# Kernel optimization log

Hardware: AMD Instinct MI355X
Metric: run time of the kernel (lower is better)

The kernel has to match this reference:

```python
import jax, jax.numpy as jnp
import numpy as np

B = 128
J = 22
Q = J * 4          # 88
R = 3
C = 4
H = 512            # LSTM hidden
ENC = 256 * 3      # 768 concatenated encoder outputs
STATE_IN = Q + R + C   # 95
OFF_IN = Q + R         # 91
OUT = Q + R + C        # 95


def _linear_params(key, fan_in, fan_out):
    kw, kb = jax.random.split(key)
    s = 1.0 / np.sqrt(fan_in)
    w = jax.random.uniform(kw, (fan_in, fan_out), jnp.float32, -s, s)
    b = jax.random.uniform(kb, (fan_out,), jnp.float32, -s, s)
    return w, b


def setup_inputs() -> dict:
    key = jax.random.key(0)
    ks = jax.random.split(key, 24)
    inp = {
        "past_root_vel": jax.random.normal(ks[0], (B, 10, R)) * 0.1,
        "past_quats": jax.random.normal(ks[1], (B, 10, Q)),
        "past_root_offset": jax.random.normal(ks[2], (B, 10, R)),
        "past_quat_offset": jax.random.normal(ks[3], (B, 10, Q)),
        "past_contacts": jax.random.uniform(ks[4], (B, 10, C)),
        "target_root_pos": jax.random.normal(ks[5], (B, R)),
        "target_quats": jax.random.normal(ks[6], (B, Q)),
        "init_root_pos": jax.random.normal(ks[7], (B, R)),
        "pred_weights": jax.random.normal(ks[8], (B, 4 * H, ENC + H)) * 0.03,
        "pred_bias": jax.random.normal(ks[9], (B, 4 * H)) * 0.01,
    }
    inp["se_w1"], inp["se_b1"] = _linear_params(ks[10], STATE_IN, 512)
    inp["se_w2"], inp["se_b2"] = _linear_params(ks[11], 512, 256)
    inp["oe_w1"], inp["oe_b1"] = _linear_params(ks[12], OFF_IN, 512)
    inp["oe_w2"], inp["oe_b2"] = _linear_params(ks[13], 512, 256)
    inp["te_w1"], inp["te_b1"] = _linear_params(ks[14], Q, 512)
    inp["te_w2"], inp["te_b2"] = _linear_params(ks[15], 512, 256)
    inp["de_w1"], inp["de_b1"] = _linear_params(ks[16], H, 512)
    inp["de_w2"], inp["de_b2"] = _linear_params(ks[17], 512, 256)
    inp["de_w3"], inp["de_b3"] = _linear_params(ks[18], 256, OUT)
    return inp


def reference(past_root_vel, past_quats, past_root_offset, past_quat_offset,
              past_contacts, target_root_pos, target_quats, init_root_pos,
              pred_weights, pred_bias,
              se_w1, se_b1, se_w2, se_b2,
              oe_w1, oe_b1, oe_w2, oe_b2,
              te_w1, te_b1, te_w2, te_b2,
              de_w1, de_b1, de_w2, de_b2, de_w3, de_b3):
    b = past_quats.shape[0]

    def enc(x, w1, b1, w2, b2):
        return jax.nn.relu(jax.nn.relu(x @ w1 + b1) @ w2 + b2)

    # target encoding is identical every step; hoist it
    h_target = enc(target_quats, te_w1, te_b1, te_w2, te_b2)

    def step(root_vel, quats, root_offset, quat_offset, contacts, h, c):
        state_vec = jnp.concatenate([contacts, quats, root_vel], axis=1)
        offset_vec = jnp.concatenate([root_offset, quat_offset], axis=1)
        h_state = enc(state_vec, se_w1, se_b1, se_w2, se_b2)
        h_offset = enc(offset_vec, oe_w1, oe_b1, oe_w2, oe_b2)
        pred_in = jnp.concatenate([h_state, h_offset, h_target], axis=1)  # [B,768]
        # per-sample hypernetwork LSTM cell (torch gate order i,f,g,o)
        z = jnp.concatenate([pred_in, h], axis=1)  # [B, 1280]
        gates = jnp.einsum('boi,bi->bo', pred_weights, z) + pred_bias
        i_g, f_g, g_g, o_g = jnp.split(gates, 4, axis=1)
        c2 = jax.nn.sigmoid(f_g) * c + jax.nn.sigmoid(i_g) * jnp.tanh(g_g)
        h2 = jax.nn.sigmoid(o_g) * jnp.tanh(c2)
        # decoder (512,512,256,out), no activation on last layer
        d = jax.nn.relu(h2 @ de_w1 + de_b1)
        d = jax.nn.relu(d @ de_w2 + de_b2)
        out = d @ de_w3 + de_b3
        next_quats = out[:, :Q] + quats
        next_rvel = out[:, Q:Q + R] + root_vel
        next_contacts = jax.nn.sigmoid(out[:, Q + R:])
        nq = next_quats.reshape(b, Q // 4, 4)
        nq = nq / jnp.maximum(jnp.linalg.norm(nq, axis=2, keepdims=True), 1e-12)
        return next_rvel, nq.reshape(b, Q), next_contacts, h2, c2

    h0 = jnp.zeros((b, H), past_quats.dtype)
    c0 = jnp.zeros((b, H), past_quats.dtype)

    def past_body(carry, x):
        glob, h, c, _, _, _, _, _ = carry
        rvel, quats, roff, qoff, cont = x
        nrv, nq, nc, h2, c2 = step(rvel, quats, roff, qoff, cont, h, c)
        glob2 = glob + rvel
        nroff = glob2 - target_root_pos
        nqoff = nq - target_quats
        return (glob2, h2, c2, nrv, nq, nc, nroff, nqoff), None

    z3 = jnp.zeros((b, R), past_quats.dtype)
    init = (init_root_pos, h0, c0, z3,
            jnp.zeros((b, Q), past_quats.dtype),
            jnp.zeros((b, C), past_quats.dtype),
            z3, jnp.zeros((b, Q), past_quats.dtype))
    xs = (jnp.swapaxes(past_root_vel, 0, 1), jnp.swapaxes(past_quats, 0, 1),
          jnp.swapaxes(past_root_offset, 0, 1), jnp.swapaxes(past_quat_offset, 0, 1),
          jnp.swapaxes(past_contacts, 0, 1))
    carry, _ = jax.lax.scan(past_body, init, xs)
    glob, h, c, nrv, nq, nc, roff, qoff = carry

    first_frame = jnp.concatenate([nrv, nq], axis=1)  # NOTE: rvel not glob, as in source

    def trans_body(carry, _):
        glob, h, c, rvel, quats, cont, roff, qoff = carry
        nrv, nq, nc, h2, c2 = step(rvel, quats, roff, qoff, cont, h, c)
        glob2 = glob + nrv
        nroff = glob2 - target_root_pos
        nqoff = nq - target_quats
        pose = jnp.concatenate([glob2, nq], axis=1)
        return (glob2, h2, c2, nrv, nq, nc, nroff, nqoff), (pose, nc)

    carry2 = (glob, h, c, nrv, nq, nc, roff, qoff)
    _, (poses, conts) = jax.lax.scan(trans_body, carry2, None, length=29)

    pred_poses = jnp.concatenate([first_frame[:, None], jnp.swapaxes(poses, 0, 1)], axis=1)
    pred_contacts = jnp.concatenate([nc[:, None], jnp.swapaxes(conts, 0, 1)], axis=1)
    return pred_poses, pred_contacts
```

## Files before the change

kernel.cpp:

```cpp
#include <hip/hip_runtime.h>
#include <hip/hip_bf16.h>
#include <math.h>

#define BATCH 128
#define QD 88
#define HDIM 512
#define ZDIM 1280
#define GDIM 2048
#define PROW 1536
#define QSTRIDE 6144
#define NPAST 10
#define NTRANS 29
#define NSTEPS (NPAST + NTRANS)
#define OUTD 95
#define POSE_ELEMS (BATCH * 30 * 91)

typedef float f32x4 __attribute__((ext_vector_type(4)));
typedef unsigned int u32x4 __attribute__((ext_vector_type(4)));

__device__ __forceinline__ float sig_(float x) { return 1.0f / (1.0f + expf(-x)); }
__device__ __forceinline__ void dot4_(const uint4 wv, const float4 zv, float& d) {
    const float4 f = *(const float4*)&wv;
    d = fmaf(f.x, zv.x, d); d = fmaf(f.y, zv.y, d);
    d = fmaf(f.z, zv.z, d); d = fmaf(f.w, zv.w, d);
}
__device__ __forceinline__ void fma4_(float4& acc, float x, const float4 w) {
    acc.x = fmaf(x, w.x, acc.x); acc.y = fmaf(x, w.y, acc.y);
    acc.z = fmaf(x, w.z, acc.z); acc.w = fmaf(x, w.w, acc.w);
}
__device__ __forceinline__ unsigned q12_(float w, float inv) {
    const unsigned u = __float2uint_rn(fmaf(w, inv, 2048.0f));
    return (u > 4095u) ? 4095u : u;
}
__device__ __forceinline__ void pack12_(const uint4 a, const uint4 b, float inv,
                                        unsigned& o0, unsigned& o1, unsigned& o2) {
    const unsigned u0 = q12_(__uint_as_float(a.x), inv), u1 = q12_(__uint_as_float(a.y), inv);
    const unsigned u2 = q12_(__uint_as_float(a.z), inv), u3 = q12_(__uint_as_float(a.w), inv);
    const unsigned u4 = q12_(__uint_as_float(b.x), inv), u5 = q12_(__uint_as_float(b.y), inv);
    const unsigned u6 = q12_(__uint_as_float(b.z), inv), u7 = q12_(__uint_as_float(b.w), inv);
    o0 = u0 | (u1 << 12) | (u2 << 24);
    o1 = (u2 >> 8) | (u3 << 4) | (u4 << 16) | (u5 << 28);
    o2 = (u5 >> 4) | (u6 << 8) | (u7 << 20);
}
__device__ __forceinline__ float dot12_(unsigned d0, unsigned d1, unsigned d2,
                                        const float4 za, const float4 zb) {
    float acc = 0.f;
    acc = fmaf((float)((int)(d0 & 0xFFFu) - 2048), za.x, acc);
    acc = fmaf((float)((int)((d0 >> 12) & 0xFFFu) - 2048), za.y, acc);
    acc = fmaf((float)((int)((d0 >> 24) | ((d1 & 0xFu) << 8)) - 2048), za.z, acc);
    acc = fmaf((float)((int)((d1 >> 4) & 0xFFFu) - 2048), za.w, acc);
    acc = fmaf((float)((int)((d1 >> 16) & 0xFFFu) - 2048), zb.x, acc);
    acc = fmaf((float)((int)((d1 >> 28) | ((d2 & 0xFFu) << 4)) - 2048), zb.y, acc);
    acc = fmaf((float)((int)((d2 >> 8) & 0xFFFu) - 2048), zb.z, acc);
    acc = fmaf((float)((int)(d2 >> 20) - 2048), zb.w, acc);
    return acc;
}
__device__ __forceinline__ float wredmax_(float m) {
    #pragma unroll
    for (int s = 32; s >= 1; s >>= 1) m = fmaxf(m, __shfl_xor(m, s, 64));
    return m;
}
__device__ __forceinline__ float amax4_(const uint4 a, float m) {
    m = fmaxf(m, fabsf(__uint_as_float(a.x))); m = fmaxf(m, fabsf(__uint_as_float(a.y)));
    m = fmaxf(m, fabsf(__uint_as_float(a.z))); m = fmaxf(m, fabsf(__uint_as_float(a.w)));
    return m;
}

__global__ void __launch_bounds__(256)
matvec0_conv(const float* __restrict__ W, const float* __restrict__ z_ws,
             const float* __restrict__ pred_bias, unsigned char* __restrict__ Wp,
             float* __restrict__ scale_ws, float* __restrict__ g_ws, float* __restrict__ g0_ws)
{
    const int b = blockIdx.x >> 5, chunk = blockIdx.x & 31;
    const int wave = threadIdx.x >> 6, lane = threadIdx.x & 63;
    const int row0 = chunk * 64 + wave * 16;
    const float* zb = z_ws + b * ZDIM;
    const float biasv = (lane < 16) ? pred_bias[b * GDIM + row0 + lane] : 0.f;
    const int l4 = lane * 4;
    const float4 z0 = *(const float4*)(zb + l4);
    const float4 z1 = *(const float4*)(zb + 256 + l4);
    const float4 zh = *(const float4*)(zb + 512 + l4);
    const float4 z3 = *(const float4*)(zb + 768 + l4);
    const float4 z4 = *(const float4*)(zb + 1024 + l4);
    const char* wb = (const char*)W + (size_t)b * GDIM * ZDIM * 4;
    char* dstB = (char*)Wp + (size_t)b * GDIM * PROW;

    #define ISSUE(p, B) { const char* a_ = wb + (size_t)(row0 + 2 * (p)) * (ZDIM * 4) + lane * 16; \
        _Pragma("unroll") for (int i = 0; i < 10; ++i) B[i] = *(const uint4*)(a_ + i * 1024); }

    uint4 bufa[10], bufb[10];
    unsigned sst[6], hst[6];
    ISSUE(0, bufa);
    #pragma unroll
    for (int p = 0; p < 8; ++p) {
        uint4* cur = (p & 1) ? bufb : bufa;
        uint4* nxt = (p & 1) ? bufa : bufb;
        if (p < 7) ISSUE(p + 1, nxt);
        float dynA = 0.f, dynB = 0.f, statA = 0.f, statB = 0.f;
        dot4_(cur[0], z0, dynA); dot4_(cur[1], z1, dynA);
        dot4_(cur[2], zh, statA);
        dot4_(cur[3], z3, dynA); dot4_(cur[4], z4, dynA);
        dot4_(cur[5], z0, dynB); dot4_(cur[6], z1, dynB);
        dot4_(cur[7], zh, statB);
        dot4_(cur[8], z3, dynB); dot4_(cur[9], z4, dynB);
        float m0 = 0.f, m1 = 0.f;
        m0 = amax4_(cur[0], m0); m0 = amax4_(cur[1], m0);
        m0 = amax4_(cur[3], m0); m0 = amax4_(cur[4], m0);
        m1 = amax4_(cur[5], m1); m1 = amax4_(cur[6], m1);
        m1 = amax4_(cur[8], m1); m1 = amax4_(cur[9], m1);
        m0 = wredmax_(m0); m1 = wredmax_(m1);
        const float s0 = m0 * (1.f / 2047.f), s1 = m1 * (1.f / 2047.f);
        const float inv0 = (m0 > 0.f) ? 2047.f / m0 : 0.f;
        const float inv1 = (m1 > 0.f) ? 2047.f / m1 : 0.f;
        unsigned s0a, s0b, s0c, h0a, h0b, h0c, s1a, s1b, s1c, h1a, h1b, h1c;
        pack12_(cur[0], cur[1], inv0, s0a, s0b, s0c);
        pack12_(cur[3], cur[4], inv0, h0a, h0b, h0c);
        pack12_(cur[5], cur[6], inv1, s1a, s1b, s1c);
        pack12_(cur[8], cur[9], inv1, h1a, h1b, h1c);
        if ((p & 1) == 0) {
            sst[0] = s0a; sst[1] = s0b; sst[2] = s0c; sst[3] = s1a; sst[4] = s1b; sst[5] = s1c;
            hst[0] = h0a; hst[1] = h0b; hst[2] = h0c; hst[3] = h1a; hst[4] = h1b; hst[5] = h1c;
        } else {
            char* base = dstB + (size_t)((row0 + 2 * p) >> 2) * QSTRIDE + lane * 16;
            u32x4 v;
            v.x = sst[0]; v.y = sst[1]; v.z = sst[2]; v.w = sst[3];
            __builtin_nontemporal_store(v, (u32x4*)(base));
            v.x = sst[4]; v.y = sst[5]; v.z = s0a; v.w = s0b;
            __builtin_nontemporal_store(v, (u32x4*)(base + 1024));
            v.x = s0c; v.y = s1a; v.z = s1b; v.w = s1c;
            __builtin_nontemporal_store(v, (u32x4*)(base + 2048));
            v.x = hst[0]; v.y = hst[1]; v.z = hst[2]; v.w = hst[3];
            __builtin_nontemporal_store(v, (u32x4*)(base + 3072));
            v.x = hst[4]; v.y = hst[5]; v.z = h0a; v.w = h0b;
            __builtin_nontemporal_store(v, (u32x4*)(base + 4096));
            v.x = h0c; v.y = h1a; v.z = h1b; v.w = h1c;
            __builtin_nontemporal_store(v, (u32x4*)(base + 5120));
        }
        if (lane == 0) { scale_ws[b * GDIM + row0 + 2 * p] = s0;
                         scale_ws[b * GDIM + row0 + 2 * p + 1] = s1; }
        float sd0 = dynA + __shfl_xor(dynA, 32);
        float sd1 = dynB + __shfl_xor(dynB, 32);
        float ud = (lane < 32) ? sd0 : sd1;
        float ss0 = statA + __shfl_xor(statA, 32);
        float ss1 = statB + __shfl_xor(statB, 32);
        float us = (lane < 32) ? ss0 : ss1;
        #pragma unroll
        for (int m = 16; m >= 1; m >>= 1) { ud += __shfl_xor(ud, m); us += __shfl_xor(us, m); }
        const float badd = __shfl(biasv, 2 * p + ((lane >= 32) ? 1 : 0), 64);
        if (lane == 0 || lane == 32) {
            const int r = row0 + 2 * p + ((lane >= 32) ? 1 : 0);
            g0_ws[b * GDIM + r] = us + badd;
            g_ws[b * GDIM + r]  = ud + us + badd;
        }
    }
    #undef ISSUE
}

__device__ __forceinline__ void redwrite_(float rA, float rB, int lane,
                                          float g0v, float scv, int idx0,
                                          float* __restrict__ dst, int drow0) {
    const float sA = rA + __shfl_xor(rA, 32);
    const float sB = rB + __shfl_xor(rB, 32);
    float u = (lane < 32) ? sA : sB;
    #pragma unroll
    for (int m = 16; m >= 1; m >>= 1) u += __shfl_xor(u, m);
    const int hilo = (lane >= 32) ? 1 : 0;
    const float badd = __shfl(g0v, idx0 + hilo, 64);
    const float srow = __shfl(scv, idx0 + hilo, 64);
    const float val = badd + srow * u;
    if (lane == 0)       dst[drow0] = val;
    else if (lane == 32) dst[drow0 + 1] = val;
}

__global__ void __launch_bounds__(256)
epass(const unsigned char* __restrict__ Wp, const float* __restrict__ enc9,
      const float* __restrict__ scale_ws, const float* __restrict__ g0_ws,
      float* __restrict__ E_ws)
{
    const int b = blockIdx.x >> 5, chunk = blockIdx.x & 31;
    const int wave = threadIdx.x >> 6, lane = threadIdx.x & 63;
    const int row0 = chunk * 64 + wave * 16;
    const int q0 = row0 >> 2;
    const int l4 = lane * 4;
    float4 eA[9], eB[9];
    #pragma unroll
    for (int s = 0; s < 9; ++s) {
        const float* eb = enc9 + ((size_t)s * BATCH + b) * 512;
        eA[s] = *(const float4*)(eb + l4);
        eB[s] = *(const float4*)(eb + 256 + l4);
    }
    const float g0v = (lane < 16) ? g0_ws[b * GDIM + row0 + lane] : 0.f;
    const float scv = (lane < 16) ? scale_ws[b * GDIM + row0 + lane] : 0.f;
    const char* wb = (const char*)Wp + (size_t)b * GDIM * PROW;

    #define ISSUE(qq, B) { const char* a_ = wb + (size_t)(q0 + (qq)) * QSTRIDE + lane * 16; \
        B[0] = __builtin_nontemporal_load((const u32x4*)(a_)); \
        B[1] = __builtin_nontemporal_load((const u32x4*)(a_ + 1024)); \
        B[2] = __builtin_nontemporal_load((const u32x4*)(a_ + 2048)); }

    u32x4 bufa[3], bufb[3];
    ISSUE(0, bufa);
    #pragma unroll
    for (int qq = 0; qq < 4; ++qq) {
        u32x4* cur = (qq & 1) ? bufb : bufa;
        u32x4* nxt = (qq & 1) ? bufa : bufb;
        if (qq < 3) ISSUE(qq + 1, nxt);
        #pragma unroll
        for (int s = 0; s < 9; ++s) {
            const float r0 = dot12_(cur[0].x, cur[0].y, cur[0].z, eA[s], eB[s]);
            const float r1 = dot12_(cur[0].w, cur[1].x, cur[1].y, eA[s], eB[s]);
            const float r2 = dot12_(cur[1].z, cur[1].w, cur[2].x, eA[s], eB[s]);
            const float r3 = dot12_(cur[2].y, cur[2].z, cur[2].w, eA[s], eB[s]);
            float* dst = E_ws + ((size_t)s * BATCH + b) * GDIM;
            redwrite_(r0, r1, lane, g0v, scv, 4 * qq,     dst, row0 + 4 * qq);
            redwrite_(r2, r3, lane, g0v, scv, 4 * qq + 2, dst, row0 + 4 * qq + 2);
        }
    }
    #undef ISSUE
}

__global__ void __launch_bounds__(256)
matvecH(const unsigned char* __restrict__ Wp, const float* __restrict__ z_ws,
        const float* __restrict__ scale_ws, const float* __restrict__ Es,
        float* __restrict__ g_ws)
{
    const int b = blockIdx.x >> 5, chunk = blockIdx.x & 31;
    const int wave = threadIdx.x >> 6, lane = threadIdx.x & 63;
    const int row0 = chunk * 64 + wave * 16;
    const int q0 = row0 >> 2;
    const float* zb = z_ws + b * ZDIM;
    const int l4 = lane * 4;
    const float4 z3 = *(const float4*)(zb + 768 + l4);
    const float4 z4 = *(const float4*)(zb + 1024 + l4);
    const float Ev  = (lane < 16) ? Es[b * GDIM + row0 + lane] : 0.f;
    const float scv = (lane < 16) ? scale_ws[b * GDIM + row0 + lane] : 0.f;
    const char* wb = (const char*)Wp + (size_t)b * GDIM * PROW;

    #define ISSUE(qq, B) { const char* a_ = wb + (size_t)(q0 + (qq)) * QSTRIDE + 3072 + lane * 16; \
        B[0] = *(const u32x4*)(a_); \
        B[1] = *(const u32x4*)(a_ + 1024); \
        B[2] = *(const u32x4*)(a_ + 2048); }

    u32x4 buf0[3], buf1[3], buf2[3];
    ISSUE(0, buf0);
    ISSUE(1, buf1);
    #pragma unroll
    for (int qq = 0; qq < 4; ++qq) {
        u32x4* cur = (qq % 3 == 0) ? buf0 : (qq % 3 == 1) ? buf1 : buf2;
        u32x4* nxt = ((qq + 2) % 3 == 0) ? buf0 : ((qq + 2) % 3 == 1) ? buf1 : buf2;
        if (qq < 2) ISSUE(qq + 2, nxt);
        const float r0 = dot12_(cur[0].x, cur[0].y, cur[0].z, z3, z4);
        const float r1 = dot12_(cur[0].w, cur[1].x, cur[1].y, z3, z4);
        const float r2 = dot12_(cur[1].z, cur[1].w, cur[2].x, z3, z4);
        const float r3 = dot12_(cur[2].y, cur[2].z, cur[2].w, z3, z4);
        float* dst = g_ws + b * GDIM;
        redwrite_(r0, r1, lane, Ev, scv, 4 * qq,     dst, row0 + 4 * qq);
        redwrite_(r2, r3, lane, Ev, scv, 4 * qq + 2, dst, row0 + 4 * qq + 2);
    }
    #undef ISSUE
}

__global__ void __launch_bounds__(256)
matvec12(const unsigned char* __restrict__ Wp, const float* __restrict__ z_ws,
         const float* __restrict__ scale_ws, const float* __restrict__ g0_ws,
         float* __restrict__ g_ws)
{
    const int b = blockIdx.x >> 5, chunk = blockIdx.x & 31;
    const int wave = threadIdx.x >> 6, lane = threadIdx.x & 63;
    const int row0 = chunk * 64 + wave * 16;
    const int q0 = row0 >> 2;
    const float* zb = z_ws + b * ZDIM;
    const int l4 = lane * 4;
    const float4 z0 = *(const float4*)(zb + l4);
    const float4 z1 = *(const float4*)(zb + 256 + l4);
    const float4 z3 = *(const float4*)(zb + 768 + l4);
    const float4 z4 = *(const float4*)(zb + 1024 + l4);
    const float g0v = (lane < 16) ? g0_ws[b * GDIM + row0 + lane] : 0.f;
    const float scv = (lane < 16) ? scale_ws[b * GDIM + row0 + lane] : 0.f;
    const char* wb = (const char*)Wp + (size_t)b * GDIM * PROW;

    #define ISSUE(qq, B) { const char* a_ = wb + (size_t)(q0 + (qq)) * QSTRIDE + lane * 16; \
        B[0] = __builtin_nontemporal_load((const u32x4*)(a_)); \
        B[1] = __builtin_nontemporal_load((const u32x4*)(a_ + 1024)); \
        B[2] = __builtin_nontemporal_load((const u32x4*)(a_ + 2048)); \
        B[3] = __builtin_nontemporal_load((const u32x4*)(a_ + 3072)); \
        B[4] = __builtin_nontemporal_load((const u32x4*)(a_ + 4096)); \
        B[5] = __builtin_nontemporal_load((const u32x4*)(a_ + 5120)); }

    u32x4 buf0[6], buf1[6], buf2[6];
    ISSUE(0, buf0);
    ISSUE(1, buf1);
    #pragma unroll
    for (int qq = 0; qq < 4; ++qq) {
        u32x4* cur = (qq % 3 == 0) ? buf0 : (qq % 3 == 1) ? buf1 : buf2;
        u32x4* nxt = ((qq + 2) % 3 == 0) ? buf0 : ((qq + 2) % 3 == 1) ? buf1 : buf2;
        if (qq < 2) ISSUE(qq + 2, nxt);
        const float r0 = dot12_(cur[0].x, cur[0].y, cur[0].z, z0, z1)
                       + dot12_(cur[3].x, cur[3].y, cur[3].z, z3, z4);
        const float r1 = dot12_(cur[0].w, cur[1].x, cur[1].y, z0, z1)
                       + dot12_(cur[3].w, cur[4].x, cur[4].y, z3, z4);
        const float r2 = dot12_(cur[1].z, cur[1].w, cur[2].x, z0, z1)
                       + dot12_(cur[4].z, cur[4].w, cur[5].x, z3, z4);
        const float r3 = dot12_(cur[2].y, cur[2].z, cur[2].w, z0, z1)
                       + dot12_(cur[5].y, cur[5].z, cur[5].w, z3, z4);
        float* dst = g_ws + b * GDIM;
        redwrite_(r0, r1, lane, g0v, scv, 4 * qq,     dst, row0 + 4 * qq);
        redwrite_(r2, r3, lane, g0v, scv, 4 * qq + 2, dst, row0 + 4 * qq + 2);
    }
    #undef ISSUE
}

__global__ void __launch_bounds__(512)
initk(const float* __restrict__ past_root_vel, const float* __restrict__ past_quats,
      const float* __restrict__ past_root_offset, const float* __restrict__ past_quat_offset,
      const float* __restrict__ past_contacts, const float* __restrict__ target_quats,
      const float* __restrict__ init_root_pos,
      const float* __restrict__ se_w1, const float* __restrict__ se_b1,
      const float* __restrict__ se_w2, const float* __restrict__ se_b2,
      const float* __restrict__ oe_w1, const float* __restrict__ oe_b1,
      const float* __restrict__ oe_w2, const float* __restrict__ oe_b2,
      const float* __restrict__ te_w1, const float* __restrict__ te_b1,
      const float* __restrict__ te_w2, const float* __restrict__ te_b2,
      float* __restrict__ z_ws, float* __restrict__ c_ws, float* __restrict__ car_ws)
{
    const int b = blockIdx.x, t = threadIdx.x;
    __shared__ float tq[QD], bufA[512], bufB[512], sv[95], ov[91];

    if (t < 192) car_ws[b * 192 + t] = (t < 3) ? init_root_pos[b * 3 + t] : 0.f;
    c_ws[b * HDIM + t] = 0.f;
    z_ws[b * ZDIM + 768 + t] = 0.f;
    if (t < QD) tq[t] = target_quats[b * QD + t];
    if (t < 4)  sv[t] = past_contacts[b * NPAST * 4 + t];
    if (t < QD) { sv[4 + t] = past_quats[b * NPAST * QD + t];
                  ov[3 + t] = past_quat_offset[b * NPAST * QD + t]; }
    if (t < 3)  { sv[92 + t] = past_root_vel[b * NPAST * 3 + t];
                  ov[t]      = past_root_offset[b * NPAST * 3 + t]; }
    __syncthreads();
    {
        float a = te_b1[t];
        #pragma unroll 8
        for (int i = 0; i < QD; ++i) a = fmaf(tq[i], te_w1[i * 512 + t], a);
        bufA[t] = fmaxf(a, 0.f);
    }
    __syncthreads();
    if (t < 256) {
        float a = te_b2[t];
        #pragma unroll 8
        for (int i = 0; i < 512; ++i) a = fmaf(bufA[i], te_w2[i * 256 + t], a);
        z_ws[b * ZDIM + 512 + t] = fmaxf(a, 0.f);
    }
    __syncthreads();
    {
        float aS = se_b1[t], aO = oe_b1[t];
        #pragma unroll 8
        for (int i = 0; i < 91; ++i) { aS = fmaf(sv[i], se_w1[i * 512 + t], aS);
                                       aO = fmaf(ov[i], oe_w1[i * 512 + t], aO); }
        #pragma unroll
        for (int i = 91; i < 95; ++i) aS = fmaf(sv[i], se_w1[i * 512 + t], aS);
        bufA[t] = fmaxf(aS, 0.f);
        bufB[t] = fmaxf(aO, 0.f);
    }
    __syncthreads();
    if (t < 256) {
        float a = se_b2[t];
        #pragma unroll 8
        for (int i = 0; i < 512; ++i) a = fmaf(bufA[i], se_w2[i * 256 + t], a);
        z_ws[b * ZDIM + t] = fmaxf(a, 0.f);
    } else {
        const int j = t - 256;
        float a = oe_b2[j];
        #pragma unroll 8
        for (int i = 0; i < 512; ++i) a = fmaf(bufB[i], oe_w2[i * 256 + j], a);
        z_ws[b * ZDIM + 256 + j] = fmaxf(a, 0.f);
    }
}

__global__ void __launch_bounds__(512)
enc_past(const float* __restrict__ past_root_vel, const float* __restrict__ past_quats,
         const float* __restrict__ past_root_offset, const float* __restrict__ past_quat_offset,
         const float* __restrict__ past_contacts,
         const float* __restrict__ se_w1, const float* __restrict__ se_b1,
         const float* __restrict__ se_w2, const float* __restrict__ se_b2,
         const float* __restrict__ oe_w1, const float* __restrict__ oe_b1,
         const float* __restrict__ oe_w2, const float* __restrict__ oe_b2,
         float* __restrict__ enc9)
{
    const int b = blockIdx.x, t = threadIdx.x;
    const int s = blockIdx.y + 1;
    __shared__ float bufA[512], bufB[512], sv[95], ov[91];

    if (t < 4)  sv[t] = past_contacts[(b * NPAST + s) * 4 + t];
    if (t < QD) { sv[4 + t] = past_quats[(b * NPAST + s) * QD + t];
                  ov[3 + t] = past_quat_offset[(b * NPAST + s) * QD + t]; }
    if (t < 3)  { sv[92 + t] = past_root_vel[(b * NPAST + s) * 3 + t];
                  ov[t]      = past_root_offset[(b * NPAST + s) * 3 + t]; }
    __syncthreads();
    {
        float aS = se_b1[t], aO = oe_b1[t];
        #pragma unroll 8
        for (int i = 0; i < 91; ++i) { aS = fmaf(sv[i], se_w1[i * 512 + t], aS);
                                       aO = fmaf(ov[i], oe_w1[i * 512 + t], aO); }
        #pragma unroll
        for (int i = 91; i < 95; ++i) aS = fmaf(sv[i], se_w1[i * 512 + t], aS);
        bufA[t] = fmaxf(aS, 0.f);
        bufB[t] = fmaxf(aO, 0.f);
    }
    __syncthreads();
    float* dst = enc9 + ((size_t)(s - 1) * BATCH + b) * 512;
    if (t < 256) {
        float a = se_b2[t];
        #pragma unroll 8
        for (int i = 0; i < 512; ++i) a = fmaf(bufA[i], se_w2[i * 256 + t], a);
        dst[t] = fmaxf(a, 0.f);
    } else {
        const int j = t - 256;
        float a = oe_b2[j];
        #pragma unroll 8
        for (int i = 0; i < 512; ++i) a = fmaf(bufB[i], oe_w2[i * 256 + j], a);
        dst[256 + j] = fmaxf(a, 0.f);
    }
}

__global__ void __launch_bounds__(512)
stepk(const float* __restrict__ past_root_vel, const float* __restrict__ past_quats,
      const float* __restrict__ past_root_offset, const float* __restrict__ past_quat_offset,
      const float* __restrict__ past_contacts, const float* __restrict__ target_root_pos,
      const float* __restrict__ target_quats,
      const float* __restrict__ se_w1, const float* __restrict__ se_b1,
      const float* __restrict__ se_w2, const float* __restrict__ se_b2,
      const float* __restrict__ oe_w1, const float* __restrict__ oe_b1,
      const float* __restrict__ oe_w2, const float* __restrict__ oe_b2,
      const float* __restrict__ de_w1, const float* __restrict__ de_b1,
      const float* __restrict__ de_w2, const float* __restrict__ de_b2,
      const float* __restrict__ de_w3, const float* __restrict__ de_b3,
      float* __restrict__ out, float* __restrict__ z_ws, const float* __restrict__ g_ws,
      float* __restrict__ c_ws, float* __restrict__ car_ws, int s, int skip_enc)
{
    const int b = blockIdx.x, t = threadIdx.x;
    __shared__ float4 part4[512];
    __shared__ __align__(16) float h2s[HDIM], bufA[512], bufB[512], d2[256];
    __shared__ float outv[OUTD], nq[QD], sv[95], ov[91], carryL[192], tq[QD], trp[3];
    __shared__ float rvn[3], globn[3], contn[4];

    if (t < 192) carryL[t] = car_ws[b * 192 + t];
    if (t < QD) tq[t] = target_quats[b * QD + t];
    if (t < 3)  trp[t] = target_root_pos[b * 3 + t];

    {
        const float* g = g_ws + b * GDIM;
        const float ig = g[t], fg = g[512 + t], gg = g[1024 + t], og = g[1536 + t];
        const float c2 = sig_(fg) * c_ws[b * HDIM + t] + sig_(ig) * tanhf(gg);
        c_ws[b * HDIM + t] = c2;
        const float h2 = sig_(og) * tanhf(c2);
        h2s[t] = h2;
        z_ws[b * ZDIM + 768 + t] = h2;
    }
    __syncthreads();
    {
        const int c = t & 127, s4 = t >> 7;
        float4 acc = {0.f, 0.f, 0.f, 0.f};
        const float* w = de_w1 + (size_t)(s4 * 128) * 512 + 4 * c;
        #pragma unroll 8
        for (int k = 0; k < 128; ++k)
            fma4_(acc, h2s[s4 * 128 + k], *(const float4*)(w + (size_t)k * 512));
        part4[t] = acc;
    }
    __syncthreads();
    if (t < 128) {
        float4 v = part4[t];
        #pragma unroll
        for (int s4 = 1; s4 < 4; ++s4) { const float4 p = part4[s4 * 128 + t];
            v.x += p.x; v.y += p.y; v.z += p.z; v.w += p.w; }
        const float4 bb = *(const float4*)(de_b1 + 4 * t);
        float4 r; r.x = fmaxf(v.x + bb.x, 0.f); r.y = fmaxf(v.y + bb.y, 0.f);
        r.z = fmaxf(v.z + bb.z, 0.f); r.w = fmaxf(v.w + bb.w, 0.f);
        *(float4*)&bufA[4 * t] = r;
    }
    __syncthreads();
    {
        const int c = t & 63, s8 = t >> 6;
        float4 acc = {0.f, 0.f, 0.f, 0.f};
        const float* w = de_w2 + (size_t)(s8 * 64) * 256 + 4 * c;
        #pragma unroll 8
        for (int k = 0; k < 64; ++k)
            fma4_(acc, bufA[s8 * 64 + k], *(const float4*)(w + (size_t)k * 256));
        part4[t] = acc;
    }
    __syncthreads();
    if (t < 64) {
        float4 v = part4[t];
        #pragma unroll
        for (int s8 = 1; s8 < 8; ++s8) { const float4 p = part4[s8 * 64 + t];
            v.x += p.x; v.y += p.y; v.z += p.z; v.w += p.w; }
        const float4 bb = *(const float4*)(de_b2 + 4 * t);
        float4 r; r.x = fmaxf(v.x + bb.x, 0.f); r.y = fmaxf(v.y + bb.y, 0.f);
        r.z = fmaxf(v.z + bb.z, 0.f); r.w = fmaxf(v.w + bb.w, 0.f);
        *(float4*)&d2[4 * t] = r;
    }
    __syncthreads();
    if (t < OUTD) {
        float acc = de_b3[t];
        #pragma unroll 16
        for (int i = 0; i < 256; ++i) acc = fmaf(d2[i], de_w3[i * OUTD + t], acc);
        outv[t] = acc;
    }
    __syncthreads();

    const bool pastS = (s < NPAST);
    if (t < QD) {
        const float qin = pastS ? past_quats[(b * NPAST + s) * QD + t] : carryL[10 + t];
        nq[t] = outv[t] + qin;
    }
    __syncthreads();
    if (t < 22) {
        const float a = nq[4 * t], b2 = nq[4 * t + 1], c3 = nq[4 * t + 2], d4 = nq[4 * t + 3];
        const float inv = 1.f / fmaxf(sqrtf(a * a + b2 * b2 + c3 * c3 + d4 * d4), 1e-12f);
        nq[4 * t] = a * inv; nq[4 * t + 1] = b2 * inv; nq[4 * t + 2] = c3 * inv; nq[4 * t + 3] = d4 * inv;
    }
    if (t < 3) {
        const float rin = pastS ? past_root_vel[(b * NPAST + s) * 3 + t] : carryL[3 + t];
        const float nrv = outv[88 + t] + rin;
        const float g = carryL[t] + (pastS ? rin : nrv);
        rvn[t] = nrv; globn[t] = g;
    }
    if (t < 4) contn[t] = sig_(outv[91 + t]);
    __syncthreads();

    if (t < 3) { car_ws[b * 192 + t] = globn[t]; car_ws[b * 192 + 3 + t] = rvn[t];
                 car_ws[b * 192 + 186 + t] = globn[t] - trp[t]; }
    if (t < 4) car_ws[b * 192 + 6 + t] = contn[t];
    if (t < QD) { car_ws[b * 192 + 10 + t] = nq[t]; car_ws[b * 192 + 98 + t] = nq[t] - tq[t]; }
    if (s == NPAST - 1) {
        const size_t pb = (size_t)b * 30 * 91;
        if (t < 3)  out[pb + t] = rvn[t];
        if (t < QD) out[pb + 3 + t] = nq[t];
        if (t < 4)  out[POSE_ELEMS + (size_t)b * 30 * 4 + t] = contn[t];
    } else if (!pastS) {
        const int k = s - NPAST + 1;
        const size_t pb = ((size_t)b * 30 + k) * 91;
        if (t < 3)  out[pb + t] = globn[t];
        if (t < QD) out[pb + 3 + t] = nq[t];
        if (t < 4)  out[POSE_ELEMS + ((size_t)b * 30 + k) * 4 + t] = contn[t];
    }
    if (s == NSTEPS - 1) return;
    if (skip_enc) return;

    const int nx = s + 1;
    if (nx < NPAST) {
        if (t < 4)  sv[t] = past_contacts[(b * NPAST + nx) * 4 + t];
        if (t < QD) { sv[4 + t] = past_quats[(b * NPAST + nx) * QD + t];
                      ov[3 + t] = past_quat_offset[(b * NPAST + nx) * QD + t]; }
        if (t < 3)  { sv[92 + t] = past_root_vel[(b * NPAST + nx) * 3 + t];
                      ov[t]      = past_root_offset[(b * NPAST + nx) * 3 + t]; }
    } else {
        if (t < 4)  sv[t] = contn[t];
        if (t < QD) { sv[4 + t] = nq[t]; ov[3 + t] = nq[t] - tq[t]; }
        if (t < 3)  { sv[92 + t] = rvn[t]; ov[t] = globn[t] - trp[t]; }
    }
    __syncthreads();
    {
        const int tt = t & 255, enc = t >> 8;
        const int c = tt & 127, sl = tt >> 7;
        const float* inp = enc ? ov : sv;
        const float* w1  = enc ? oe_w1 : se_w1;
        const int nin  = enc ? 91 : 95;
        const int half = enc ? 46 : 48;
        const int i0 = sl * half;
        const int iend = (i0 + half < nin) ? (i0 + half) : nin;
        float4 acc = {0.f, 0.f, 0.f, 0.f};
        #pragma unroll 8
        for (int k = 0; k < 48; ++k) {
            const int i = i0 + k;
            if (i < iend) fma4_(acc, inp[i], *(const float4*)(w1 + (size_t)i * 512 + 4 * c));
        }
        part4[enc * 256 + tt] = acc;
    }
    __syncthreads();
    if (t < 128) {
        const float4 a = part4[t], b2 = part4[128 + t];
        const float4 bb = *(const float4*)(se_b1 + 4 * t);
        float4 r; r.x = fmaxf(a.x + b2.x + bb.x, 0.f); r.y = fmaxf(a.y + b2.y + bb.y, 0.f);
        r.z = fmaxf(a.z + b2.z + bb.z, 0.f); r.w = fmaxf(a.w + b2.w + bb.w, 0.f);
        *(float4*)&bufA[4 * t] = r;
    } else if (t < 256) {
        const int c = t - 128;
        const float4 a = part4[256 + c], b2 = part4[384 + c];
        const float4 bb = *(const float4*)(oe_b1 + 4 * c);
        float4 r; r.x = fmaxf(a.x + b2.x + bb.x, 0.f); r.y = fmaxf(a.y + b2.y + bb.y, 0.f);
        r.z = fmaxf(a.z + b2.z + bb.z, 0.f); r.w = fmaxf(a.w + b2.w + bb.w, 0.f);
        *(float4*)&bufB[4 * c] = r;
    }
    __syncthreads();
    {
        const int tt = t & 255, enc = t >> 8;
        const int c = tt & 63, sl = tt >> 6;
        const float* inp = enc ? bufB : bufA;
        const float* w2  = enc ? oe_w2 : se_w2;
        float4 acc = {0.f, 0.f, 0.f, 0.f};
        const float* w = w2 + (size_t)(sl * 128) * 256 + 4 * c;
        #pragma unroll 8
        for (int k = 0; k < 128; ++k)
            fma4_(acc, inp[sl * 128 + k], *(const float4*)(w + (size_t)k * 256));
        part4[enc * 256 + tt] = acc;
    }
    __syncthreads();
    if (t < 64) {
        float4 v = part4[t];
        #pragma unroll
        for (int sl = 1; sl < 4; ++sl) { const float4 p = part4[sl * 64 + t];
            v.x += p.x; v.y += p.y; v.z += p.z; v.w += p.w; }
        const float4 bb = *(const float4*)(se_b2 + 4 * t);
        float4 r; r.x = fmaxf(v.x + bb.x, 0.f); r.y = fmaxf(v.y + bb.y, 0.f);
        r.z = fmaxf(v.z + bb.z, 0.f); r.w = fmaxf(v.w + bb.w, 0.f);
        *(float4*)(z_ws + b * ZDIM + 4 * t) = r;
    } else if (t < 128) {
        const int c = t - 64;
        float4 v = part4[256 + c];
        #pragma unroll
        for (int sl = 1; sl < 4; ++sl) { const float4 p = part4[256 + sl * 64 + c];
            v.x += p.x; v.y += p.y; v.z += p.z; v.w += p.w; }
        const float4 bb = *(const float4*)(oe_b2 + 4 * c);
        float4 r; r.x = fmaxf(v.x + bb.x, 0.f); r.y = fmaxf(v.y + bb.y, 0.f);
        r.z = fmaxf(v.z + bb.z, 0.f); r.w = fmaxf(v.w + bb.w, 0.f);
        *(float4*)(z_ws + b * ZDIM + 256 + 4 * c) = r;
    }
}

__global__ void __launch_bounds__(256)
matvec_f32(const float* __restrict__ W, const float* __restrict__ z_ws,
           const float* __restrict__ pred_bias, float* __restrict__ g_ws)
{
    const int b = blockIdx.x >> 5, chunk = blockIdx.x & 31;
    const int wave = threadIdx.x >> 6, lane = threadIdx.x & 63;
    const int row0 = chunk * 64 + wave * 16;
    const float* zb = z_ws + b * ZDIM;
    const float biasv = (lane < 16) ? pred_bias[b * GDIM + row0 + lane] : 0.f;
    const int l4 = lane * 4;
    const float4 z0 = *(const float4*)(zb + l4);
    const float4 z1 = *(const float4*)(zb + 256 + l4);
    const float4 z2 = *(const float4*)(zb + 512 + l4);
    const float4 z3 = *(const float4*)(zb + 768 + l4);
    const float4 z4 = *(const float4*)(zb + 1024 + l4);
    const char* wb = (const char*)W + (size_t)b * GDIM * ZDIM * 4;

    #define ISSUE(p, B) { const char* a_ = wb + (size_t)(row0 + 2 * (p)) * (ZDIM * 4) + lane * 16; \
        _Pragma("unroll") for (int i = 0; i < 10; ++i) B[i] = *(const uint4*)(a_ + i * 1024); }

    uint4 bufa[10], bufb[10];
    ISSUE(0, bufa);
    #pragma unroll
    for (int p = 0; p < 8; ++p) {
        uint4* cur = (p & 1) ? bufb : bufa;
        uint4* nxt = (p & 1) ? bufa : bufb;
        if (p < 7) ISSUE(p + 1, nxt);
        float accA = 0.f, accB = 0.f;
        dot4_(cur[0], z0, accA); dot4_(cur[1], z1, accA); dot4_(cur[2], z2, accA);
        dot4_(cur[3], z3, accA); dot4_(cur[4], z4, accA);
        dot4_(cur[5], z0, accB); dot4_(cur[6], z1, accB); dot4_(cur[7], z2, accB);
        dot4_(cur[8], z3, accB); dot4_(cur[9], z4, accB);
        float s0 = accA + __shfl_xor(accA, 32);
        float s1 = accB + __shfl_xor(accB, 32);
        float u = (lane < 32) ? s0 : s1;
        #pragma unroll
        for (int m = 16; m >= 1; m >>= 1) u += __shfl_xor(u, m);
        const float badd = __shfl(biasv, 2 * p + ((lane >= 32) ? 1 : 0), 64);
        if (lane == 0)       g_ws[b * GDIM + row0 + 2 * p]     = u + badd;
        else if (lane == 32) g_ws[b * GDIM + row0 + 2 * p + 1] = u + badd;
    }
    #undef ISSUE
}

extern "C" void kernel_launch(void* const* d_in, const int* in_sizes, int n_in,
                              void* d_out, int out_size, void* d_ws, size_t ws_size,
                              hipStream_t stream) {
    const float* prv = (const float*)d_in[0];
    const float* pq  = (const float*)d_in[1];
    const float* pro = (const float*)d_in[2];
    const float* pqo = (const float*)d_in[3];
    const float* pc  = (const float*)d_in[4];
    const float* trp = (const float*)d_in[5];
    const float* tq  = (const float*)d_in[6];
    const float* irp = (const float*)d_in[7];
    const float* pw  = (const float*)d_in[8];
    const float* pb  = (const float*)d_in[9];
    const float* se_w1 = (const float*)d_in[10]; const float* se_b1 = (const float*)d_in[11];
    const float* se_w2 = (const float*)d_in[12]; const float* se_b2 = (const float*)d_in[13];
    const float* oe_w1 = (const float*)d_in[14]; const float* oe_b1 = (const float*)d_in[15];
    const float* oe_w2 = (const float*)d_in[16]; const float* oe_b2 = (const float*)d_in[17];
    const float* te_w1 = (const float*)d_in[18]; const float* te_b1 = (const float*)d_in[19];
    const float* te_w2 = (const float*)d_in[20]; const float* te_b2 = (const float*)d_in[21];
    const float* de_w1 = (const float*)d_in[22]; const float* de_b1 = (const float*)d_in[23];
    const float* de_w2 = (const float*)d_in[24]; const float* de_b2 = (const float*)d_in[25];
    const float* de_w3 = (const float*)d_in[26]; const float* de_b3 = (const float*)d_in[27];
    float* outp = (float*)d_out;

    const size_t WPACKB = (size_t)BATCH * GDIM * PROW;
    const size_t AUXB = (size_t)BATCH * (GDIM * 3 + ZDIM + HDIM + 192) * 4
                      + (size_t)9 * BATCH * 512 * 4
                      + (size_t)9 * BATCH * GDIM * 4;
    const bool bf = ws_size >= WPACKB + AUXB;

    char* base = (char*)d_ws;
    float* scale_ws; float* g0_ws; float* z_ws;
    if (bf) {
        scale_ws = (float*)(base + WPACKB);
        g0_ws    = scale_ws + (size_t)BATCH * GDIM;
        z_ws     = g0_ws + (size_t)BATCH * GDIM;
    } else {
        scale_ws = nullptr;
        g0_ws    = nullptr;
        z_ws     = (float*)base;
    }
    float* g_ws    = z_ws + (size_t)BATCH * ZDIM;
    float* c_ws    = g_ws + (size_t)BATCH * GDIM;
    float* car_ws  = c_ws + (size_t)BATCH * HDIM;
    float* enc9_ws = car_ws + (size_t)BATCH * 192;
    float* E_ws    = enc9_ws + (size_t)9 * BATCH * 512;

    initk<<<dim3(BATCH), dim3(512), 0, stream>>>(prv, pq, pro, pqo, pc, tq, irp,
        se_w1, se_b1, se_w2, se_b2, oe_w1, oe_b1, oe_w2, oe_b2,
        te_w1, te_b1, te_w2, te_b2, z_ws, c_ws, car_ws);

    if (bf) {
        enc_past<<<dim3(BATCH, 9), dim3(512), 0, stream>>>(prv, pq, pro, pqo, pc,
            se_w1, se_b1, se_w2, se_b2, oe_w1, oe_b1, oe_w2, oe_b2, enc9_ws);
        matvec0_conv<<<dim3(BATCH * 32), dim3(256), 0, stream>>>(
            pw, z_ws, pb, (unsigned char*)d_ws, scale_ws, g_ws, g0_ws);
        epass<<<dim3(BATCH * 32), dim3(256), 0, stream>>>(
            (const unsigned char*)d_ws, enc9_ws, scale_ws, g0_ws, E_ws);
        for (int s = 0; s < NSTEPS; ++s) {
            if (s >= 1 && s < NPAST) {
                matvecH<<<dim3(BATCH * 32), dim3(256), 0, stream>>>(
                    (const unsigned char*)d_ws, z_ws, scale_ws,
                    E_ws + (size_t)(s - 1) * BATCH * GDIM, g_ws);
            } else if (s >= NPAST) {
                matvec12<<<dim3(BATCH * 32), dim3(256), 0, stream>>>(
                    (const unsigned char*)d_ws, z_ws, scale_ws, g0_ws, g_ws);
            }
            const int skip_enc = (s + 1 < NPAST) ? 1 : 0;
            stepk<<<dim3(BATCH), dim3(512), 0, stream>>>(prv, pq, pro, pqo, pc, trp, tq,
                se_w1, se_b1, se_w2, se_b2, oe_w1, oe_b1, oe_w2, oe_b2,
                de_w1, de_b1, de_w2, de_b2, de_w3, de_b3,
                outp, z_ws, g_ws, c_ws, car_ws, s, skip_enc);
        }
    } else {
        for (int s = 0; s < NSTEPS; ++s) {
            matvec_f32<<<dim3(BATCH * 32), dim3(256), 0, stream>>>(pw, z_ws, pb, g_ws);
            stepk<<<dim3(BATCH), dim3(512), 0, stream>>>(prv, pq, pro, pqo, pc, trp, tq,
                se_w1, se_b1, se_w2, se_b2, oe_w1, oe_b1, oe_w2, oe_b2,
                de_w1, de_b1, de_w2, de_b2, de_w3, de_b3,
                outp, z_ws, g_ws, c_ws, car_ws, s, 0);
        }
    }
}
```

Before: 4.261 ms.

## Replace early past-step kernels with a lightweight LSTM-only kernel

For the first nine past steps, the full step kernel (decoder MLP and state updates) is replaced with a small kernel that only applies the LSTM cell update. The accumulated root position for those steps is precomputed in the init kernel by summing past root velocities. This removes decoder and encoder work whose outputs are overwritten during the past frames. Separately, the matvec weight loads switch from nontemporal to ordinary loads, which changes cache behaviour. The risk is that some side state from the skipped steps (contacts, offsets) is actually needed later.

```diff
diff --git a/kernel.cpp b/kernel.cpp
--- a/kernel.cpp
+++ b/kernel.cpp
@@ -280,12 +280,12 @@
     const char* wb = (const char*)Wp + (size_t)b * GDIM * PROW;
 
     #define ISSUE(qq, B) { const char* a_ = wb + (size_t)(q0 + (qq)) * QSTRIDE + lane * 16; \
-        B[0] = __builtin_nontemporal_load((const u32x4*)(a_)); \
-        B[1] = __builtin_nontemporal_load((const u32x4*)(a_ + 1024)); \
-        B[2] = __builtin_nontemporal_load((const u32x4*)(a_ + 2048)); \
-        B[3] = __builtin_nontemporal_load((const u32x4*)(a_ + 3072)); \
-        B[4] = __builtin_nontemporal_load((const u32x4*)(a_ + 4096)); \
-        B[5] = __builtin_nontemporal_load((const u32x4*)(a_ + 5120)); }
+        B[0] = *(const u32x4*)(a_); \
+        B[1] = *(const u32x4*)(a_ + 1024); \
+        B[2] = *(const u32x4*)(a_ + 2048); \
+        B[3] = *(const u32x4*)(a_ + 3072); \
+        B[4] = *(const u32x4*)(a_ + 4096); \
+        B[5] = *(const u32x4*)(a_ + 5120); }
 
     u32x4 buf0[6], buf1[6], buf2[6];
     ISSUE(0, buf0);
@@ -311,6 +311,17 @@
 }
 
 __global__ void __launch_bounds__(512)
+lstmk(const float* __restrict__ g_ws, float* __restrict__ z_ws, float* __restrict__ c_ws)
+{
+    const int b = blockIdx.x, t = threadIdx.x;
+    const float* g = g_ws + b * GDIM;
+    const float ig = g[t], fg = g[512 + t], gg = g[1024 + t], og = g[1536 + t];
+    const float c2 = sig_(fg) * c_ws[b * HDIM + t] + sig_(ig) * tanhf(gg);
+    c_ws[b * HDIM + t] = c2;
+    z_ws[b * ZDIM + 768 + t] = sig_(og) * tanhf(c2);
+}
+
+__global__ void __launch_bounds__(512)
 initk(const float* __restrict__ past_root_vel, const float* __restrict__ past_quats,
       const float* __restrict__ past_root_offset, const float* __restrict__ past_quat_offset,
       const float* __restrict__ past_contacts, const float* __restrict__ target_quats,
@@ -326,7 +337,14 @@
     const int b = blockIdx.x, t = threadIdx.x;
     __shared__ float tq[QD], bufA[512], bufB[512], sv[95], ov[91];
 
-    if (t < 192) car_ws[b * 192 + t] = (t < 3) ? init_root_pos[b * 3 + t] : 0.f;
+    if (t < 192) {
+        float v = 0.f;
+        if (t < 3) {
+            v = init_root_pos[b * 3 + t];
+            for (int s = 0; s < NPAST - 1; ++s) v += past_root_vel[(b * NPAST + s) * 3 + t];
+        }
+        car_ws[b * 192 + t] = v;
+    }
     c_ws[b * HDIM + t] = 0.f;
     z_ws[b * ZDIM + 768 + t] = 0.f;
     if (t < QD) tq[t] = target_quats[b * QD + t];
@@ -737,11 +755,14 @@
                 matvec12<<<dim3(BATCH * 32), dim3(256), 0, stream>>>(
                     (const unsigned char*)d_ws, z_ws, scale_ws, g0_ws, g_ws);
             }
-            const int skip_enc = (s + 1 < NPAST) ? 1 : 0;
-            stepk<<<dim3(BATCH), dim3(512), 0, stream>>>(prv, pq, pro, pqo, pc, trp, tq,
-                se_w1, se_b1, se_w2, se_b2, oe_w1, oe_b1, oe_w2, oe_b2,
-                de_w1, de_b1, de_w2, de_b2, de_w3, de_b3,
-                outp, z_ws, g_ws, c_ws, car_ws, s, skip_enc);
+            if (s < NPAST - 1) {
+                lstmk<<<dim3(BATCH), dim3(512), 0, stream>>>(g_ws, z_ws, c_ws);
+            } else {
+                stepk<<<dim3(BATCH), dim3(512), 0, stream>>>(prv, pq, pro, pqo, pc, trp, tq,
+                    se_w1, se_b1, se_w2, se_b2, oe_w1, oe_b1, oe_w2, oe_b2,
+                    de_w1, de_b1, de_w2, de_b2, de_w3, de_b3,
+                    outp, z_ws, g_ws, c_ws, car_ws, s, 0);
+            }
         }
     } else {
         for (int s = 0; s < NSTEPS; ++s) {
```

Measured after the change: 5.009 ms. +17.5%, slower.
